# Kernel tuning notes

Measured on AMD Instinct MI355X. Metric: run time of the kernel, lower is better.

## Reference

```python
import jax, jax.numpy as jnp
import numpy as np

B, LQ, LK, D = 32, 2048, 2048, 256
TEMPERATURE = 16.0  # sqrt(D)
MASK_P = 0.15


def setup_inputs() -> dict:
    key = jax.random.key(0)
    kq, kk, kv, ks, km = jax.random.split(key, 5)
    q = jax.random.normal(kq, (B, LQ, D), dtype=jnp.float32)
    k = jax.random.normal(kk, (B, LK, D), dtype=jnp.float32)
    v = jax.random.normal(kv, (B, LK, D), dtype=jnp.float32)
    # random boolean masks (True = masked); low density so no row is fully masked
    src_mask = jax.random.bernoulli(ks, MASK_P, (B, LQ, LK))
    mel_mask = jax.random.bernoulli(km, MASK_P, (B, LQ, LK))
    return {"q": q, "k": k, "v": v, "src_mask": src_mask, "mel_mask": mel_mask}


def reference(q, k, v, src_mask, mel_mask):
    # attn = (q @ k^T) / temperature, shape [B, LQ, LK]
    attn = jnp.einsum("bqd,bkd->bqk", q, k) / TEMPERATURE
    # dual-mask path: mel_mask -> -inf before softmax, src_mask -> 0 after softmax
    attn = jnp.where(mel_mask, -jnp.inf, attn)
    attn = jax.nn.softmax(attn, axis=2)
    attn = jnp.where(src_mask, 0.0, attn)
    output = jnp.einsum("bqk,bkd->bqd", attn, v)
    return (output, attn)
```

## Files before the change

### kernel.cpp

```cpp
#include <hip/hip_runtime.h>
#include <hip/hip_bf16.h>
#include <cstdint>

#define B_   32
#define LQ_  2048
#define LK_  2048
#define D_   256
#define INV_T 0.0625f

typedef __attribute__((ext_vector_type(8))) short bf16x8;
typedef __attribute__((ext_vector_type(4))) float f32x4;

__device__ __forceinline__ unsigned short f2bf(float f) {
    union { float f; unsigned u; } a; a.f = f;
    unsigned u = a.u;
    unsigned r = (u + 0x7FFFu + ((u >> 16) & 1u)) >> 16;
    return (unsigned short)r;
}

__device__ __forceinline__ unsigned long long pack4bf(float a, float b, float c, float d) {
    return (unsigned long long)f2bf(a)
         | ((unsigned long long)f2bf(b) << 16)
         | ((unsigned long long)f2bf(c) << 32)
         | ((unsigned long long)f2bf(d) << 48);
}

__global__ __launch_bounds__(256) void qk_exp_kernel(
    const float* __restrict__ q, const float* __restrict__ kmat,
    const int* __restrict__ mel, float* __restrict__ attn,
    float* __restrict__ rowsum)
{
    const int b  = blockIdx.z;
    const int m0 = blockIdx.y * 128;
    const int n0 = blockIdx.x * 128;

    __shared__ unsigned short As[128][72];
    __shared__ unsigned short Bs[128][72];

    const int tid  = threadIdx.x;
    const int wave = tid >> 6, lane = tid & 63;
    const int wm   = wave >> 1, wn = wave & 1;
    const int quad = lane >> 4, l16 = lane & 15;

    f32x4 acc[4][4];
#pragma unroll
    for (int i = 0; i < 4; ++i)
#pragma unroll
        for (int j = 0; j < 4; ++j) acc[i][j] = (f32x4)(0.0f);

    const float* qb = q    + (size_t)b * LQ_ * D_;
    const float* kb = kmat + (size_t)b * LK_ * D_;

    const int sr = tid >> 4;
    const int sc = (tid & 15) * 4;

    for (int kt = 0; kt < 4; ++kt) {
        const int kbase = kt * 64;
#pragma unroll
        for (int p = 0; p < 8; ++p) {
            const int row = sr + p * 16;
            float4 va = *(const float4*)&qb[(size_t)(m0 + row) * D_ + kbase + sc];
            float4 vb = *(const float4*)&kb[(size_t)(n0 + row) * D_ + kbase + sc];
            As[row][sc+0] = f2bf(va.x); As[row][sc+1] = f2bf(va.y);
            As[row][sc+2] = f2bf(va.z); As[row][sc+3] = f2bf(va.w);
            Bs[row][sc+0] = f2bf(vb.x); Bs[row][sc+1] = f2bf(vb.y);
            Bs[row][sc+2] = f2bf(vb.z); Bs[row][sc+3] = f2bf(vb.w);
        }
        __syncthreads();
#pragma unroll
        for (int ks = 0; ks < 2; ++ks) {
            bf16x8 af[4], bfr[4];
#pragma unroll
            for (int i = 0; i < 4; ++i)
                af[i] = *(const bf16x8*)&As[wm*64 + i*16 + l16][ks*32 + quad*8];
#pragma unroll
            for (int j = 0; j < 4; ++j)
                bfr[j] = *(const bf16x8*)&Bs[wn*64 + j*16 + l16][ks*32 + quad*8];
#pragma unroll
            for (int i = 0; i < 4; ++i)
#pragma unroll
                for (int j = 0; j < 4; ++j)
                    acc[i][j] = __builtin_amdgcn_mfma_f32_16x16x32_bf16(
                        af[i], bfr[j], acc[i][j], 0, 0, 0);
        }
        __syncthreads();
    }

    float*      attnB = attn + (size_t)b * LQ_ * LK_;
    const int*  melB  = mel  + (size_t)b * LQ_ * LK_;

    float rs[4][4];
#pragma unroll
    for (int i = 0; i < 4; ++i)
#pragma unroll
        for (int r = 0; r < 4; ++r) rs[i][r] = 0.0f;

#pragma unroll
    for (int i = 0; i < 4; ++i) {
#pragma unroll
        for (int j = 0; j < 4; ++j) {
#pragma unroll
            for (int r = 0; r < 4; ++r) {
                const int row = wm*64 + i*16 + quad*4 + r;
                const int col = wn*64 + j*16 + l16;
                const size_t gi = (size_t)(m0 + row) * LK_ + (n0 + col);
                float s = acc[i][j][r] * INV_T;
                float p = melB[gi] ? 0.0f : __expf(s);
                attnB[gi] = p;
                rs[i][r] += p;
            }
        }
    }

#pragma unroll
    for (int i = 0; i < 4; ++i) {
#pragma unroll
        for (int r = 0; r < 4; ++r) {
            float s = rs[i][r];
            s += __shfl_xor(s, 1);
            s += __shfl_xor(s, 2);
            s += __shfl_xor(s, 4);
            s += __shfl_xor(s, 8);
            if (l16 == 0) {
                const int row = wm*64 + i*16 + quad*4 + r;
                atomicAdd(&rowsum[(size_t)b * LQ_ + m0 + row], s);
            }
        }
    }
}


__device__ __forceinline__ const bf16x8* lds_frag(
    const unsigned short (*arr)[64], int row, int chunk) {
    const int key = (row ^ (row >> 3)) & 7;
    return (const bf16x8*)&arr[row][(chunk ^ key) << 3];
}

__device__ __forceinline__ int swz8(int row, int e) {
    return (e & 7) | ((((e >> 3) ^ row ^ (row >> 3)) & 7) << 3);
}

__global__ __launch_bounds__(256, 4) void pv_norm_kernel(
    const float* __restrict__ v, const int* __restrict__ src,
    const float* __restrict__ rowsum, float* __restrict__ attn,
    float* __restrict__ out)
{
    const int b  = blockIdx.y;
    const int m0 = blockIdx.x * 64;

    __shared__ unsigned short As[64][64];
    __shared__ unsigned short Vt[256][64];

    const int tid  = threadIdx.x;
    const int wave = tid >> 6, lane = tid & 63;
    const int wn   = wave;
    const int quad = lane >> 4, l16 = lane & 15;

    f32x4 acc[4][4];
#pragma unroll
    for (int i = 0; i < 4; ++i)
#pragma unroll
        for (int j = 0; j < 4; ++j) acc[i][j] = (f32x4)(0.0f);

    const float* vb    = v    + (size_t)b * LK_ * D_;
    float*       attnB = attn + (size_t)b * LQ_ * LK_;
    const int*   srcB  = src  + (size_t)b * LQ_ * LK_;

    const int sr = tid >> 4;
    const int sc = (tid & 15) * 4;

    float il[4];
#pragma unroll
    for (int p = 0; p < 4; ++p)
        il[p] = 1.0f / rowsum[(size_t)b * LQ_ + m0 + sr + p * 16];

    for (int kt = 0; kt < 32; ++kt) {
        const int k0 = kt * 64;

#pragma unroll
        for (int p = 0; p < 4; ++p) {
            const int row = sr + p * 16;
            const size_t gi = (size_t)(m0 + row) * LK_ + k0 + sc;
            float4 pv = *(const float4*)&attnB[gi];
            int4   sv = *(const int4*)&srcB[gi];
            const float ilp = il[p];
            float a0 = sv.x ? 0.0f : pv.x * ilp;
            float a1 = sv.y ? 0.0f : pv.y * ilp;
            float a2 = sv.z ? 0.0f : pv.z * ilp;
            float a3 = sv.w ? 0.0f : pv.w * ilp;
            float4 st; st.x = a0; st.y = a1; st.z = a2; st.w = a3;
            *(float4*)&attnB[gi] = st;
            *(unsigned long long*)&As[row][swz8(row, sc)] = pack4bf(a0, a1, a2, a3);
        }

#pragma unroll
        for (int p = 0; p < 4; ++p) {
            const int bi  = tid + p * 256;
            const int bkv = (bi >> 6) * 4;
            const int bn  = (bi & 63) * 4;
            const float* s0 = &vb[(size_t)(k0 + bkv) * D_ + bn];
            float4 r0 = *(const float4*)(s0);
            float4 r1 = *(const float4*)(s0 + D_);
            float4 r2 = *(const float4*)(s0 + 2 * D_);
            float4 r3 = *(const float4*)(s0 + 3 * D_);
            *(unsigned long long*)&Vt[bn+0][swz8(bn+0, bkv)] = pack4bf(r0.x, r1.x, r2.x, r3.x);
            *(unsigned long long*)&Vt[bn+1][swz8(bn+1, bkv)] = pack4bf(r0.y, r1.y, r2.y, r3.y);
            *(unsigned long long*)&Vt[bn+2][swz8(bn+2, bkv)] = pack4bf(r0.z, r1.z, r2.z, r3.z);
            *(unsigned long long*)&Vt[bn+3][swz8(bn+3, bkv)] = pack4bf(r0.w, r1.w, r2.w, r3.w);
        }
        __syncthreads();

#pragma unroll
        for (int ks = 0; ks < 2; ++ks) {
            bf16x8 af[4], bfr[4];
            const int chunk = ks * 4 + quad;
#pragma unroll
            for (int i = 0; i < 4; ++i)
                af[i] = *lds_frag(As, i*16 + l16, chunk);
#pragma unroll
            for (int j = 0; j < 4; ++j)
                bfr[j] = *lds_frag(Vt, wn*64 + j*16 + l16, chunk);
#pragma unroll
            for (int i = 0; i < 4; ++i)
#pragma unroll
                for (int j = 0; j < 4; ++j)
                    acc[i][j] = __builtin_amdgcn_mfma_f32_16x16x32_bf16(
                        af[i], bfr[j], acc[i][j], 0, 0, 0);
        }
        __syncthreads();
    }

    float* outB = out + (size_t)b * LQ_ * D_;
#pragma unroll
    for (int i = 0; i < 4; ++i) {
#pragma unroll
        for (int j = 0; j < 4; ++j) {
#pragma unroll
            for (int r = 0; r < 4; ++r) {
                const int row = i*16 + quad*4 + r;
                const int col = wn*64 + j*16 + l16;
                outB[(size_t)(m0 + row) * D_ + col] = acc[i][j][r];
            }
        }
    }
}

extern "C" void kernel_launch(void* const* d_in, const int* in_sizes, int n_in,
                              void* d_out, int out_size, void* d_ws, size_t ws_size,
                              hipStream_t stream) {
    const float* q        = (const float*)d_in[0];
    const float* k        = (const float*)d_in[1];
    const float* v        = (const float*)d_in[2];
    const int*   src_mask = (const int*)d_in[3];
    const int*   mel_mask = (const int*)d_in[4];

    float* out  = (float*)d_out;
    float* attn = out + (size_t)B_ * LQ_ * D_;
    float* rowsum = (float*)d_ws;

    hipMemsetAsync(rowsum, 0, (size_t)B_ * LQ_ * sizeof(float), stream);

    qk_exp_kernel<<<dim3(LK_/128, LQ_/128, B_), 256, 0, stream>>>(
        q, k, mel_mask, attn, rowsum);

    pv_norm_kernel<<<dim3(LQ_/64, B_), 256, 0, stream>>>(
        v, src_mask, rowsum, attn, out);
}
```

Baseline: 2.016 ms.

## Remap blocks per XCD by batch and prefetch next attn/src tile in PV kernel

Both kernels now use a flat 1D grid whose block index is remapped so each batch's tiles land on the same XCD (block id mod 8). The intent is to keep a batch's K/V and Q data in that XCD's L2. The PV kernel also register-prefetches the next attn and src_mask tile before the barrier, to overlap global loads with the MFMA work. Its launch bound drops the minimum-occupancy hint of 4, which raises register headroom for the prefetch at the cost of possibly lower occupancy.

```diff
diff --git a/kernel.cpp b/kernel.cpp
--- a/kernel.cpp
+++ b/kernel.cpp
@@ -30,9 +30,13 @@
     const int* __restrict__ mel, float* __restrict__ attn,
     float* __restrict__ rowsum)
 {
-    const int b  = blockIdx.z;
-    const int m0 = blockIdx.y * 128;
-    const int n0 = blockIdx.x * 128;
+    const int id  = blockIdx.x;
+    const int xcd = id & 7;
+    const int idx = id >> 3;
+    const int b   = xcd + 8 * (idx >> 8);
+    const int t   = idx & 255;
+    const int m0  = (t >> 4) * 128;
+    const int n0  = (t & 15) * 128;
 
     __shared__ unsigned short As[128][72];
     __shared__ unsigned short Bs[128][72];
@@ -140,13 +144,16 @@
     return (e & 7) | ((((e >> 3) ^ row ^ (row >> 3)) & 7) << 3);
 }
 
-__global__ __launch_bounds__(256, 4) void pv_norm_kernel(
+__global__ __launch_bounds__(256) void pv_norm_kernel(
     const float* __restrict__ v, const int* __restrict__ src,
     const float* __restrict__ rowsum, float* __restrict__ attn,
     float* __restrict__ out)
 {
-    const int b  = blockIdx.y;
-    const int m0 = blockIdx.x * 64;
+    const int id  = blockIdx.x;
+    const int xcd = id & 7;
+    const int idx = id >> 3;
+    const int b   = xcd + 8 * (idx >> 5);
+    const int m0  = (idx & 31) * 64;
 
     __shared__ unsigned short As[64][64];
     __shared__ unsigned short Vt[256][64];
@@ -174,6 +181,15 @@
     for (int p = 0; p < 4; ++p)
         il[p] = 1.0f / rowsum[(size_t)b * LQ_ + m0 + sr + p * 16];
 
+    float4 pv_r[4]; int4 sv_r[4];
+#pragma unroll
+    for (int p = 0; p < 4; ++p) {
+        const int row = sr + p * 16;
+        const size_t gi = (size_t)(m0 + row) * LK_ + sc;
+        pv_r[p] = *(const float4*)&attnB[gi];
+        sv_r[p] = *(const int4*)&srcB[gi];
+    }
+
     for (int kt = 0; kt < 32; ++kt) {
         const int k0 = kt * 64;
 
@@ -181,13 +197,11 @@
         for (int p = 0; p < 4; ++p) {
             const int row = sr + p * 16;
             const size_t gi = (size_t)(m0 + row) * LK_ + k0 + sc;
-            float4 pv = *(const float4*)&attnB[gi];
-            int4   sv = *(const int4*)&srcB[gi];
             const float ilp = il[p];
-            float a0 = sv.x ? 0.0f : pv.x * ilp;
-            float a1 = sv.y ? 0.0f : pv.y * ilp;
-            float a2 = sv.z ? 0.0f : pv.z * ilp;
-            float a3 = sv.w ? 0.0f : pv.w * ilp;
+            float a0 = sv_r[p].x ? 0.0f : pv_r[p].x * ilp;
+            float a1 = sv_r[p].y ? 0.0f : pv_r[p].y * ilp;
+            float a2 = sv_r[p].z ? 0.0f : pv_r[p].z * ilp;
+            float a3 = sv_r[p].w ? 0.0f : pv_r[p].w * ilp;
             float4 st; st.x = a0; st.y = a1; st.z = a2; st.w = a3;
             *(float4*)&attnB[gi] = st;
             *(unsigned long long*)&As[row][swz8(row, sc)] = pack4bf(a0, a1, a2, a3);
@@ -208,6 +222,16 @@
             *(unsigned long long*)&Vt[bn+2][swz8(bn+2, bkv)] = pack4bf(r0.z, r1.z, r2.z, r3.z);
             *(unsigned long long*)&Vt[bn+3][swz8(bn+3, bkv)] = pack4bf(r0.w, r1.w, r2.w, r3.w);
         }
+
+        if (kt < 31) {
+#pragma unroll
+            for (int p = 0; p < 4; ++p) {
+                const int row = sr + p * 16;
+                const size_t gi = (size_t)(m0 + row) * LK_ + (k0 + 64) + sc;
+                pv_r[p] = *(const float4*)&attnB[gi];
+                sv_r[p] = *(const int4*)&srcB[gi];
+            }
+        }
         __syncthreads();
 
 #pragma unroll
@@ -260,9 +284,9 @@
 
     hipMemsetAsync(rowsum, 0, (size_t)B_ * LQ_ * sizeof(float), stream);
 
-    qk_exp_kernel<<<dim3(LK_/128, LQ_/128, B_), 256, 0, stream>>>(
+    qk_exp_kernel<<<dim3(16 * 16 * B_), 256, 0, stream>>>(
         q, k, mel_mask, attn, rowsum);
 
-    pv_norm_kernel<<<dim3(LQ_/64, B_), 256, 0, stream>>>(
+    pv_norm_kernel<<<dim3((LQ_ / 64) * B_), 256, 0, stream>>>(
         v, src_mask, rowsum, attn, out);
 }
```

Result: faster. 1.734 ms (-14.0%).
